# Optimization experiments

Hardware: AMD Instinct MI355X
Metric: run time of the kernel (lower is better)

## Reference

```python
import jax, jax.numpy as jnp
import numpy as np

N = 16384
C = 128
F = 128

def setup_inputs() -> dict:
    key = jax.random.key(0)
    k1, k2, k3, k4 = jax.random.split(key, 4)
    X = jax.random.normal(k1, (N, C), dtype=jnp.float32)
    adj = jax.random.uniform(k2, (N, N), dtype=jnp.float32)
    W = jax.random.normal(k3, (C, F), dtype=jnp.float32) * 0.05
    b = jax.random.normal(k4, (F,), dtype=jnp.float32) * 0.05
    return {"X": X, "adj": adj, "W": W, "b": b}

def reference(X, adj, W, b):
    # adj_hat = adj + I (self-loops)
    adj_hat = adj + jnp.eye(adj.shape[0], dtype=adj.dtype)
    # D^{-1/2}: inverse of sqrt of the diagonal degree matrix == 1/sqrt(rowsum)
    d_inv_sqrt = 1.0 / jnp.sqrt(jnp.sum(adj_hat, axis=1))  # [N]
    # Symmetric normalization via row/col scaling (same math as D^-1/2 @ A @ D^-1/2)
    adj_norm = adj_hat * d_inv_sqrt[:, None] * d_inv_sqrt[None, :]
    # Feature transform first (N*C*F) then aggregate (N*N*F)
    out = adj_norm @ (X @ W) + b
    return jax.nn.relu(out)
```

## Files before the change

kernel.cpp:

```cpp
#include <hip/hip_runtime.h>
#include <hip/hip_bf16.h>

typedef __attribute__((ext_vector_type(8))) short short8;
typedef __attribute__((ext_vector_type(4))) float f32x4;

#define N_NODES 16384
#define FEAT 128
#define NT 256

__device__ __forceinline__ short f2bf(float x) {
  union { float f; unsigned u; } v;
  v.f = x;
  unsigned r = v.u + 0x7fffu + ((v.u >> 16) & 1u);
  return (short)(r >> 16);
}

__global__ __launch_bounds__(256) void rowsum_kernel(
    const float* __restrict__ adj, float* __restrict__ dinv)
{
  const int row = blockIdx.x;
  const float4* p4 = (const float4*)(adj + (size_t)row * N_NODES);
  float s = 0.f;
  #pragma unroll 4
  for (int i = threadIdx.x; i < N_NODES / 4; i += 256) {
    float4 v = p4[i];
    s += (v.x + v.y) + (v.z + v.w);
  }
  #pragma unroll
  for (int off = 32; off > 0; off >>= 1) s += __shfl_down(s, off, 64);
  __shared__ float part[4];
  if ((threadIdx.x & 63) == 0) part[threadIdx.x >> 6] = s;
  __syncthreads();
  if (threadIdx.x == 0) {
    float tot = (part[0] + part[1]) + (part[2] + part[3]) + 1.0f;
    dinv[row] = rsqrtf(tot);
  }
}

__global__ __launch_bounds__(256) void xw_kernel(
    const float* __restrict__ X, const float* __restrict__ W,
    const float* __restrict__ dinv,
    __hip_bfloat16* __restrict__ Ynat, __hip_bfloat16* __restrict__ Ypack)
{
  __shared__ __align__(16) float Ws[64][128];
  __shared__ __align__(16) float Xs[32][128];
  __shared__ __align__(16) short Ts[128][40];
  const int tid = threadIdx.x;
  const int row0 = blockIdx.x << 5;

  {
    const float4* Xg = (const float4*)(X + ((size_t)row0 << 7));
    float4* Xl = (float4*)&Xs[0][0];
    #pragma unroll
    for (int i = 0; i < 4; ++i) Xl[tid + (i << 8)] = Xg[tid + (i << 8)];
  }
  const int f  = tid & 127;
  const int rr = tid >> 7;
  float acc[16];
  #pragma unroll
  for (int k = 0; k < 16; ++k) acc[k] = 0.f;

  for (int cc = 0; cc < 2; ++cc) {
    __syncthreads();
    {
      const float4* Wg = (const float4*)(W + ((size_t)cc << 13));
      float4* Wl = (float4*)&Ws[0][0];
      #pragma unroll
      for (int i = 0; i < 8; ++i) Wl[tid + (i << 8)] = Wg[tid + (i << 8)];
    }
    __syncthreads();
    for (int c4 = 0; c4 < 16; ++c4) {
      const int cl = c4 << 2;
      const float w0 = Ws[cl + 0][f];
      const float w1 = Ws[cl + 1][f];
      const float w2 = Ws[cl + 2][f];
      const float w3 = Ws[cl + 3][f];
      const int cg = (cc << 6) + cl;
      #pragma unroll
      for (int k = 0; k < 16; ++k) {
        const float4 x = *(const float4*)&Xs[rr + (k << 1)][cg];
        acc[k] += x.x * w0 + x.y * w1 + x.z * w2 + x.w * w3;
      }
    }
  }
  #pragma unroll
  for (int k = 0; k < 16; ++k) {
    const int r = rr + (k << 1);
    const float dv = dinv[row0 + r];
    const short v = f2bf(acc[k] * dv);
    ((short*)Ynat)[(size_t)(row0 + r) * FEAT + f] = v;
    Ts[f][r] = v;
  }
  __syncthreads();
  {
    const int f2 = tid >> 1;
    const int h  = (tid & 1) << 4;
    const short8 v0 = *(const short8*)&Ts[f2][h];
    const short8 v1 = *(const short8*)&Ts[f2][h + 8];
    short* o = (short*)Ypack;
    *(short8*)(o + (size_t)(row0 + h) * FEAT + (f2 << 3))     = v0;
    *(short8*)(o + (size_t)(row0 + h + 8) * FEAT + (f2 << 3)) = v1;
  }
}

#define SPMM_BODY(T, BCUR, BNXT, ALD0, ALD1, AST0, AST1, RD, WR)               \
  {                                                                            \
    if ((T) + 2 < NT) {           \
      const float* ap = Ag + (((T) + 2) << 6);                                 \
      ALD0 = *(const float4*)(ap);                                             \
      ALD1 = *(const float4*)(ap + 4);                                         \
    }                                                                          \
    if ((T) + 1 < NT) {  \
      const short* yp0 = Yg + (((T) + 1) << 13);                               \
      const short* yp1 = yp0 + 4096;                                           \
      BNXT[0] = *(const short8*)(yp0);                                         \
      BNXT[1] = *(const short8*)(yp0 + 128);                                   \
      BNXT[2] = *(const short8*)(yp0 + 256);                                   \
      BNXT[3] = *(const short8*)(yp0 + 384);                                   \
      BNXT[4] = *(const short8*)(yp1);                                         \
      BNXT[5] = *(const short8*)(yp1 + 128);                                   \
      BNXT[6] = *(const short8*)(yp1 + 256);                                   \
      BNXT[7] = *(const short8*)(yp1 + 384);                                   \
    }                                                                          \
    {                                                                          \
      const short8 af0 = *(const short8*)&As[RD][(wm << 4) + lm][lk];          \
      acc[0] = __builtin_amdgcn_mfma_f32_16x16x32_bf16(af0, BCUR[0], acc[0], 0, 0, 0); \
      acc[1] = __builtin_amdgcn_mfma_f32_16x16x32_bf16(af0, BCUR[1], acc[1], 0, 0, 0); \
      acc[2] = __builtin_amdgcn_mfma_f32_16x16x32_bf16(af0, BCUR[2], acc[2], 0, 0, 0); \
      acc[3] = __builtin_amdgcn_mfma_f32_16x16x32_bf16(af0, BCUR[3], acc[3], 0, 0, 0); \
      const short8 af1 = *(const short8*)&As[RD][(wm << 4) + lm][32 + lk];     \
      acc[0] = __builtin_amdgcn_mfma_f32_16x16x32_bf16(af1, BCUR[4], acc[0], 0, 0, 0); \
      acc[1] = __builtin_amdgcn_mfma_f32_16x16x32_bf16(af1, BCUR[5], acc[1], 0, 0, 0); \
      acc[2] = __builtin_amdgcn_mfma_f32_16x16x32_bf16(af1, BCUR[6], acc[2], 0, 0, 0); \
      acc[3] = __builtin_amdgcn_mfma_f32_16x16x32_bf16(af1, BCUR[7], acc[3], 0, 0, 0); \
    }                                                                          \
    if ((T) + 1 < NT) {  \
      short8 ac;                                                               \
      ac[0] = f2bf(AST0.x); ac[1] = f2bf(AST0.y);                              \
      ac[2] = f2bf(AST0.z); ac[3] = f2bf(AST0.w);                              \
      ac[4] = f2bf(AST1.x); ac[5] = f2bf(AST1.y);                              \
      ac[6] = f2bf(AST1.z); ac[7] = f2bf(AST1.w);                              \
      *(short8*)&As[WR][ar][ak] = ac;                                          \
    }                                                                          \
    __syncthreads();                                                           \
  }

__global__ __launch_bounds__(512, 2) void spmm_kernel(
    const float* __restrict__ A,
    const __hip_bfloat16* __restrict__ Ynat,
    const __hip_bfloat16* __restrict__ Ypack,
    const float* __restrict__ dinv,
    const float* __restrict__ bias,
    float* __restrict__ out)
{
  __shared__ __align__(16) short As[2][64][72];
  const int tid  = threadIdx.x;
  const int row0 = blockIdx.x << 6;

  const int ar = tid >> 3;
  const int ak = (tid & 7) << 3;
  const float* Ag = A + (size_t)(row0 + ar) * N_NODES + ak;

  const int wid  = tid >> 6;
  const int wm   = wid >> 1;
  const int wf   = wid & 1;
  const int lane = tid & 63;
  const int lm   = lane & 15;
  const int lk   = (lane >> 4) << 3;

  const short* Yg = (const short*)Ypack + (lk << 7) + (wf << 9) + (lm << 3);

  f32x4 acc[4];
  #pragma unroll
  for (int c = 0; c < 4; ++c) acc[c] = (f32x4){0.f, 0.f, 0.f, 0.f};

  float4 aA0, aA1, aB0, aB1;
  short8 b0[8], b1[8];

  aA0 = *(const float4*)(Ag);
  aA1 = *(const float4*)(Ag + 4);
  aB0 = *(const float4*)(Ag + 64);
  aB1 = *(const float4*)(Ag + 68);
  {
    const short* yp0 = Yg;
    const short* yp1 = Yg + 4096;
    b0[0] = *(const short8*)(yp0);
    b0[1] = *(const short8*)(yp0 + 128);
    b0[2] = *(const short8*)(yp0 + 256);
    b0[3] = *(const short8*)(yp0 + 384);
    b0[4] = *(const short8*)(yp1);
    b0[5] = *(const short8*)(yp1 + 128);
    b0[6] = *(const short8*)(yp1 + 256);
    b0[7] = *(const short8*)(yp1 + 384);
  }
  {
    short8 ac;
    ac[0] = f2bf(aA0.x); ac[1] = f2bf(aA0.y); ac[2] = f2bf(aA0.z); ac[3] = f2bf(aA0.w);
    ac[4] = f2bf(aA1.x); ac[5] = f2bf(aA1.y); ac[6] = f2bf(aA1.z); ac[7] = f2bf(aA1.w);
    *(short8*)&As[0][ar][ak] = ac;
  }
  __syncthreads();

  for (int t = 0; t < NT; t += 2) {
    SPMM_BODY(t,     b0, b1, aA0, aA1, aB0, aB1, 0, 1)
    SPMM_BODY(t + 1, b1, b0, aB0, aB1, aA0, aA1, 1, 0)
  }

  const int lr = (lane >> 4) << 2;
  float dreg[4];
  #pragma unroll
  for (int r = 0; r < 4; ++r) dreg[r] = dinv[row0 + (wm << 4) + lr + r];
  #pragma unroll
  for (int c = 0; c < 4; ++c) {
    const int col = (wf << 6) + (c << 4) + lm;
    const float bv = bias[col];
    #pragma unroll
    for (int r = 0; r < 4; ++r) {
      const int row = row0 + (wm << 4) + lr + r;
      const float y = __bfloat162float(Ynat[(size_t)row * FEAT + col]);
      const float v = dreg[r] * (acc[c][r] + y) + bv;
      out[(size_t)row * FEAT + col] = v > 0.f ? v : 0.f;
    }
  }
}

extern "C" void kernel_launch(void* const* d_in, const int* in_sizes, int n_in,
                              void* d_out, int out_size, void* d_ws, size_t ws_size,
                              hipStream_t stream) {
  const float* X   = (const float*)d_in[0];
  const float* adj = (const float*)d_in[1];
  const float* W   = (const float*)d_in[2];
  const float* b   = (const float*)d_in[3];
  float* out = (float*)d_out;

  float* dinv = (float*)d_ws;
  __hip_bfloat16* Ynat  = (__hip_bfloat16*)((char*)d_ws + (1 << 16));
  __hip_bfloat16* Ypack = (__hip_bfloat16*)((char*)d_ws + (1 << 16) + (1 << 22));

  rowsum_kernel<<<N_NODES, 256, 0, stream>>>(adj, dinv);
  xw_kernel<<<N_NODES / 32, 256, 0, stream>>>(X, W, dinv, Ynat, Ypack);
  spmm_kernel<<<N_NODES / 64, 512, 0, stream>>>(adj, Ynat, Ypack, dinv, b, out);
}
```

Before: 487.4 us.

## Load adjacency fragments directly into MFMA registers, fold self-loop into A, drop Ynat

The spmm kernel no longer stages the adjacency tile through LDS with per-tile barriers. Each lane now loads its own MFMA A-fragment straight from global memory and converts it to bf16 in registers. The identity self-loop is added into the adjacency fragment on the diagonal tile, so the separate Ynat buffer and its epilogue reads go away. The rowsum kernel changes to one wave per row with no shared-memory reduction. The trade-off is that the adjacency global loads are now less coalesced (each lane reads 32-byte pieces at a row stride) and the bf16 conversion work is duplicated across the waves that share rows.

```diff
diff --git a/kernel.cpp b/kernel.cpp
--- a/kernel.cpp
+++ b/kernel.cpp
@@ -18,29 +18,25 @@
 __global__ __launch_bounds__(256) void rowsum_kernel(
     const float* __restrict__ adj, float* __restrict__ dinv)
 {
-  const int row = blockIdx.x;
-  const float4* p4 = (const float4*)(adj + (size_t)row * N_NODES);
+  const int w    = threadIdx.x >> 6;
+  const int lane = threadIdx.x & 63;
+  const int row  = (blockIdx.x << 2) + w;
+  const float4* p4 = (const float4*)(adj + (size_t)row * N_NODES) + lane;
   float s = 0.f;
-  #pragma unroll 4
-  for (int i = threadIdx.x; i < N_NODES / 4; i += 256) {
-    float4 v = p4[i];
+  #pragma unroll 8
+  for (int it = 0; it < 64; ++it) {
+    float4 v = p4[it << 6];
     s += (v.x + v.y) + (v.z + v.w);
   }
   #pragma unroll
   for (int off = 32; off > 0; off >>= 1) s += __shfl_down(s, off, 64);
-  __shared__ float part[4];
-  if ((threadIdx.x & 63) == 0) part[threadIdx.x >> 6] = s;
-  __syncthreads();
-  if (threadIdx.x == 0) {
-    float tot = (part[0] + part[1]) + (part[2] + part[3]) + 1.0f;
-    dinv[row] = rsqrtf(tot);
-  }
+  if (lane == 0) dinv[row] = rsqrtf(s + 1.0f);
 }
 
 __global__ __launch_bounds__(256) void xw_kernel(
     const float* __restrict__ X, const float* __restrict__ W,
     const float* __restrict__ dinv,
-    __hip_bfloat16* __restrict__ Ynat, __hip_bfloat16* __restrict__ Ypack)
+    __hip_bfloat16* __restrict__ Ypack)
 {
   __shared__ __align__(16) float Ws[64][128];
   __shared__ __align__(16) float Xs[32][128];
@@ -87,9 +83,7 @@
   for (int k = 0; k < 16; ++k) {
     const int r = rr + (k << 1);
     const float dv = dinv[row0 + r];
-    const short v = f2bf(acc[k] * dv);
-    ((short*)Ynat)[(size_t)(row0 + r) * FEAT + f] = v;
-    Ts[f][r] = v;
+    Ts[f][r] = f2bf(acc[k] * dv);
   }
   __syncthreads();
   {
@@ -103,63 +97,63 @@
   }
 }
 
-#define SPMM_BODY(T, BCUR, BNXT, ALD0, ALD1, AST0, AST1, RD, WR)               \
+#define SPMM_BODY(T, A0, A1, A2, A3, NA0, NA1, NA2, NA3, BC, BN)               \
   {                                                                            \
-    if ((T) + 2 < NT) {           \
-      const float* ap = Ag + (((T) + 2) << 6);                                 \
-      ALD0 = *(const float4*)(ap);                                             \
-      ALD1 = *(const float4*)(ap + 4);                                         \
+    if ((T) + 1 < NT) {                                                        \
+      const float* ap = Ar + (((T) + 1) << 6);                                 \
+      NA0 = *(const float4*)(ap);                                              \
+      NA1 = *(const float4*)(ap + 4);                                          \
+      NA2 = *(const float4*)(ap + 32);                                         \
+      NA3 = *(const float4*)(ap + 36);                                         \
+      const short* yp = Yg + (((T) + 1) << 13);                                \
+      BN[0] = *(const short8*)(yp);                                            \
+      BN[1] = *(const short8*)(yp + 128);                                      \
+      BN[2] = *(const short8*)(yp + 256);                                      \
+      BN[3] = *(const short8*)(yp + 384);                                      \
+      BN[4] = *(const short8*)(yp + 4096);                                     \
+      BN[5] = *(const short8*)(yp + 4224);                                     \
+      BN[6] = *(const short8*)(yp + 4352);                                     \
+      BN[7] = *(const short8*)(yp + 4480);                                     \
     }                                                                          \
-    if ((T) + 1 < NT) {  \
-      const short* yp0 = Yg + (((T) + 1) << 13);                               \
-      const short* yp1 = yp0 + 4096;                                           \
-      BNXT[0] = *(const short8*)(yp0);                                         \
-      BNXT[1] = *(const short8*)(yp0 + 128);                                   \
-      BNXT[2] = *(const short8*)(yp0 + 256);                                   \
-      BNXT[3] = *(const short8*)(yp0 + 384);                                   \
-      BNXT[4] = *(const short8*)(yp1);                                         \
-      BNXT[5] = *(const short8*)(yp1 + 128);                                   \
-      BNXT[6] = *(const short8*)(yp1 + 256);                                   \
-      BNXT[7] = *(const short8*)(yp1 + 384);                                   \
+    if ((T) == bid) {     \
+      A0.x += (dp0 == 0) ? 1.0f : 0.0f;  A0.y += (dp0 == 1) ? 1.0f : 0.0f;     \
+      A0.z += (dp0 == 2) ? 1.0f : 0.0f;  A0.w += (dp0 == 3) ? 1.0f : 0.0f;     \
+      A1.x += (dp0 == 4) ? 1.0f : 0.0f;  A1.y += (dp0 == 5) ? 1.0f : 0.0f;     \
+      A1.z += (dp0 == 6) ? 1.0f : 0.0f;  A1.w += (dp0 == 7) ? 1.0f : 0.0f;     \
+      A2.x += (dp1 == 0) ? 1.0f : 0.0f;  A2.y += (dp1 == 1) ? 1.0f : 0.0f;     \
+      A2.z += (dp1 == 2) ? 1.0f : 0.0f;  A2.w += (dp1 == 3) ? 1.0f : 0.0f;     \
+      A3.x += (dp1 == 4) ? 1.0f : 0.0f;  A3.y += (dp1 == 5) ? 1.0f : 0.0f;     \
+      A3.z += (dp1 == 6) ? 1.0f : 0.0f;  A3.w += (dp1 == 7) ? 1.0f : 0.0f;     \
     }                                                                          \
     {                                                                          \
-      const short8 af0 = *(const short8*)&As[RD][(wm << 4) + lm][lk];          \
-      acc[0] = __builtin_amdgcn_mfma_f32_16x16x32_bf16(af0, BCUR[0], acc[0], 0, 0, 0); \
-      acc[1] = __builtin_amdgcn_mfma_f32_16x16x32_bf16(af0, BCUR[1], acc[1], 0, 0, 0); \
-      acc[2] = __builtin_amdgcn_mfma_f32_16x16x32_bf16(af0, BCUR[2], acc[2], 0, 0, 0); \
-      acc[3] = __builtin_amdgcn_mfma_f32_16x16x32_bf16(af0, BCUR[3], acc[3], 0, 0, 0); \
-      const short8 af1 = *(const short8*)&As[RD][(wm << 4) + lm][32 + lk];     \
-      acc[0] = __builtin_amdgcn_mfma_f32_16x16x32_bf16(af1, BCUR[4], acc[0], 0, 0, 0); \
-      acc[1] = __builtin_amdgcn_mfma_f32_16x16x32_bf16(af1, BCUR[5], acc[1], 0, 0, 0); \
-      acc[2] = __builtin_amdgcn_mfma_f32_16x16x32_bf16(af1, BCUR[6], acc[2], 0, 0, 0); \
-      acc[3] = __builtin_amdgcn_mfma_f32_16x16x32_bf16(af1, BCUR[7], acc[3], 0, 0, 0); \
+      short8 af0, af1;                                                         \
+      af0[0] = f2bf(A0.x); af0[1] = f2bf(A0.y); af0[2] = f2bf(A0.z);           \
+      af0[3] = f2bf(A0.w); af0[4] = f2bf(A1.x); af0[5] = f2bf(A1.y);           \
+      af0[6] = f2bf(A1.z); af0[7] = f2bf(A1.w);                                \
+      af1[0] = f2bf(A2.x); af1[1] = f2bf(A2.y); af1[2] = f2bf(A2.z);           \
+      af1[3] = f2bf(A2.w); af1[4] = f2bf(A3.x); af1[5] = f2bf(A3.y);           \
+      af1[6] = f2bf(A3.z); af1[7] = f2bf(A3.w);                                \
+      acc[0] = __builtin_amdgcn_mfma_f32_16x16x32_bf16(af0, BC[0], acc[0], 0, 0, 0); \
+      acc[1] = __builtin_amdgcn_mfma_f32_16x16x32_bf16(af0, BC[1], acc[1], 0, 0, 0); \
+      acc[2] = __builtin_amdgcn_mfma_f32_16x16x32_bf16(af0, BC[2], acc[2], 0, 0, 0); \
+      acc[3] = __builtin_amdgcn_mfma_f32_16x16x32_bf16(af0, BC[3], acc[3], 0, 0, 0); \
+      acc[0] = __builtin_amdgcn_mfma_f32_16x16x32_bf16(af1, BC[4], acc[0], 0, 0, 0); \
+      acc[1] = __builtin_amdgcn_mfma_f32_16x16x32_bf16(af1, BC[5], acc[1], 0, 0, 0); \
+      acc[2] = __builtin_amdgcn_mfma_f32_16x16x32_bf16(af1, BC[6], acc[2], 0, 0, 0); \
+      acc[3] = __builtin_amdgcn_mfma_f32_16x16x32_bf16(af1, BC[7], acc[3], 0, 0, 0); \
     }                                                                          \
-    if ((T) + 1 < NT) {  \
-      short8 ac;                                                               \
-      ac[0] = f2bf(AST0.x); ac[1] = f2bf(AST0.y);                              \
-      ac[2] = f2bf(AST0.z); ac[3] = f2bf(AST0.w);                              \
-      ac[4] = f2bf(AST1.x); ac[5] = f2bf(AST1.y);                              \
-      ac[6] = f2bf(AST1.z); ac[7] = f2bf(AST1.w);                              \
-      *(short8*)&As[WR][ar][ak] = ac;                                          \
-    }                                                                          \
-    __syncthreads();                                                           \
   }
 
 __global__ __launch_bounds__(512, 2) void spmm_kernel(
     const float* __restrict__ A,
-    const __hip_bfloat16* __restrict__ Ynat,
     const __hip_bfloat16* __restrict__ Ypack,
     const float* __restrict__ dinv,
     const float* __restrict__ bias,
     float* __restrict__ out)
 {
-  __shared__ __align__(16) short As[2][64][72];
   const int tid  = threadIdx.x;
-  const int row0 = blockIdx.x << 6;
-
-  const int ar = tid >> 3;
-  const int ak = (tid & 7) << 3;
-  const float* Ag = A + (size_t)(row0 + ar) * N_NODES + ak;
+  const int bid  = blockIdx.x;
+  const int row0 = bid << 6;
 
   const int wid  = tid >> 6;
   const int wm   = wid >> 1;
@@ -167,43 +161,36 @@
   const int lane = tid & 63;
   const int lm   = lane & 15;
   const int lk   = (lane >> 4) << 3;
-
+  const int myrow = (wm << 4) + lm;
+  const int dp0 = myrow - lk;
+  const int dp1 = myrow - 32 - lk;
+
+  const float* Ar = A + (size_t)(row0 + myrow) * N_NODES + lk;
   const short* Yg = (const short*)Ypack + (lk << 7) + (wf << 9) + (lm << 3);
 
   f32x4 acc[4];
   #pragma unroll
   for (int c = 0; c < 4; ++c) acc[c] = (f32x4){0.f, 0.f, 0.f, 0.f};
 
-  float4 aA0, aA1, aB0, aB1;
+  float4 aA0, aA1, aA2, aA3, aB0, aB1, aB2, aB3;
   short8 b0[8], b1[8];
 
-  aA0 = *(const float4*)(Ag);
-  aA1 = *(const float4*)(Ag + 4);
-  aB0 = *(const float4*)(Ag + 64);
-  aB1 = *(const float4*)(Ag + 68);
-  {
-    const short* yp0 = Yg;
-    const short* yp1 = Yg + 4096;
-    b0[0] = *(const short8*)(yp0);
-    b0[1] = *(const short8*)(yp0 + 128);
-    b0[2] = *(const short8*)(yp0 + 256);
-    b0[3] = *(const short8*)(yp0 + 384);
-    b0[4] = *(const short8*)(yp1);
-    b0[5] = *(const short8*)(yp1 + 128);
-    b0[6] = *(const short8*)(yp1 + 256);
-    b0[7] = *(const short8*)(yp1 + 384);
-  }
-  {
-    short8 ac;
-    ac[0] = f2bf(aA0.x); ac[1] = f2bf(aA0.y); ac[2] = f2bf(aA0.z); ac[3] = f2bf(aA0.w);
-    ac[4] = f2bf(aA1.x); ac[5] = f2bf(aA1.y); ac[6] = f2bf(aA1.z); ac[7] = f2bf(aA1.w);
-    *(short8*)&As[0][ar][ak] = ac;
-  }
-  __syncthreads();
+  aA0 = *(const float4*)(Ar);
+  aA1 = *(const float4*)(Ar + 4);
+  aA2 = *(const float4*)(Ar + 32);
+  aA3 = *(const float4*)(Ar + 36);
+  b0[0] = *(const short8*)(Yg);
+  b0[1] = *(const short8*)(Yg + 128);
+  b0[2] = *(const short8*)(Yg + 256);
+  b0[3] = *(const short8*)(Yg + 384);
+  b0[4] = *(const short8*)(Yg + 4096);
+  b0[5] = *(const short8*)(Yg + 4224);
+  b0[6] = *(const short8*)(Yg + 4352);
+  b0[7] = *(const short8*)(Yg + 4480);
 
   for (int t = 0; t < NT; t += 2) {
-    SPMM_BODY(t,     b0, b1, aA0, aA1, aB0, aB1, 0, 1)
-    SPMM_BODY(t + 1, b1, b0, aB0, aB1, aA0, aA1, 1, 0)
+    SPMM_BODY(t,     aA0, aA1, aA2, aA3, aB0, aB1, aB2, aB3, b0, b1)
+    SPMM_BODY(t + 1, aB0, aB1, aB2, aB3, aA0, aA1, aA2, aA3, b1, b0)
   }
 
   const int lr = (lane >> 4) << 2;
@@ -217,8 +204,7 @@
     #pragma unroll
     for (int r = 0; r < 4; ++r) {
       const int row = row0 + (wm << 4) + lr + r;
-      const float y = __bfloat162float(Ynat[(size_t)row * FEAT + col]);
-      const float v = dreg[r] * (acc[c][r] + y) + bv;
+      const float v = dreg[r] * acc[c][r] + bv;
       out[(size_t)row * FEAT + col] = v > 0.f ? v : 0.f;
     }
   }
@@ -234,10 +220,9 @@
   float* out = (float*)d_out;
 
   float* dinv = (float*)d_ws;
-  __hip_bfloat16* Ynat  = (__hip_bfloat16*)((char*)d_ws + (1 << 16));
-  __hip_bfloat16* Ypack = (__hip_bfloat16*)((char*)d_ws + (1 << 16) + (1 << 22));
-
-  rowsum_kernel<<<N_NODES, 256, 0, stream>>>(adj, dinv);
-  xw_kernel<<<N_NODES / 32, 256, 0, stream>>>(X, W, dinv, Ynat, Ypack);
-  spmm_kernel<<<N_NODES / 64, 512, 0, stream>>>(adj, Ynat, Ypack, dinv, b, out);
-}
+  __hip_bfloat16* Ypack = (__hip_bfloat16*)((char*)d_ws + (1 << 16));
+
+  rowsum_kernel<<<N_NODES / 4, 256, 0, stream>>>(adj, dinv);
+  xw_kernel<<<N_NODES / 32, 256, 0, stream>>>(X, W, dinv, Ypack);
+  spmm_kernel<<<N_NODES / 64, 512, 0, stream>>>(adj, Ypack, dinv, b, out);
+}
```

New measurement: 639.5 us. 1.31x slower.
